# Optimization experiments

Measured on AMD Instinct MI355X. Metric: run time of the kernel, lower is better.

Reference implementation:

```python
import jax, jax.numpy as jnp
import numpy as np
import math

B, H, L, DK = 4, 12, 1024, 64
GLOBAL, LOCAL, INIT_VAL = 8, 4, 8
W = INIT_VAL + 1  # window length fed to each GRU
MAX_VAL = 1.0e12


def setup_inputs() -> dict:
    k0 = jax.random.key(0)
    ks = jax.random.split(k0, 9)
    bound = 1.0 / math.sqrt(DK)
    uni = lambda k, shape: jax.random.uniform(k, shape, jnp.float32, -bound, bound)
    return {
        "query": jax.random.normal(ks[0], (B, H, L, DK), jnp.float32),
        "key": jax.random.normal(ks[1], (B, H, L, DK), jnp.float32),
        "value": jax.random.normal(ks[2], (B, H, L, DK), jnp.float32),
        "mask": jax.random.randint(ks[3], (B, 1, L, L), 0, 2, jnp.int32),
        # per-local-head GRU parameters (torch nn.GRU layout: gates [r, z, n])
        "w_ih": uni(ks[4], (LOCAL, 3 * DK, DK)),
        "w_hh": uni(ks[5], (LOCAL, 3 * DK, DK)),
        "b_ih": uni(ks[6], (LOCAL, 3 * DK)),
        "b_hh": uni(ks[7], (LOCAL, 3 * DK)),
    }


def reference(query, key, value, mask, w_ih, w_hh, b_ih, b_hh):
    b, h, l, d_k = query.shape
    # ---- global softmax-attention heads ----
    q_g, k_g, v_g = query[:, :GLOBAL], key[:, :GLOBAL], value[:, :GLOBAL]
    scores = jnp.einsum('bhqd,bhkd->bhqk', q_g, k_g) / math.sqrt(d_k)
    scores = jnp.where(mask == 0, -MAX_VAL, scores)
    p_attn = jax.nn.softmax(scores, axis=-1)
    out_g = jnp.einsum('bhqk,bhkd->bhqd', p_attn, v_g)  # (b, GLOBAL, l, d_k)

    # ---- local heads: windowed value gather ----
    v_l = value[:, GLOBAL:]                                   # (b, LOCAL, l, d_k)
    v_pad = jnp.pad(v_l, ((0, 0), (0, 0), (0, INIT_VAL), (0, 0)))
    dist = jnp.arange(l)[:, None] + jnp.arange(W)[None, :]    # (l, W) forward window
    v_aug = v_pad[:, :, dist, :]                              # (b, LOCAL, l, W, d_k)
    x = v_aug.reshape(b * LOCAL * l, W, d_k)                  # all windows, shared by every GRU

    # ---- per-head GRU over the window; keep last hidden state ----
    def gru_last_hidden(wih, whh, bih, bhh):
        xg = jnp.einsum('ntd,gd->ntg', x, wih) + bih          # (N, W, 3*d_k), input gates precomputed
        def step(hc, xg_t):
            gh = hc @ whh.T + bhh
            xr, xz, xn = jnp.split(xg_t, 3, axis=-1)
            hr, hz, hn = jnp.split(gh, 3, axis=-1)
            r = jax.nn.sigmoid(xr + hr)
            z = jax.nn.sigmoid(xz + hz)
            n_ = jnp.tanh(xn + r * hn)
            return (1.0 - z) * n_ + z * hc, None
        h0 = jnp.zeros((x.shape[0], d_k), x.dtype)
        hT, _ = jax.lax.scan(step, h0, jnp.swapaxes(xg, 0, 1))
        return hT                                             # (N, d_k)

    hs = jax.vmap(gru_last_hidden)(w_ih, w_hh, b_ih, b_hh)    # (LOCAL, N, d_k)
    # faithful to torch cat: GRU i applied to ALL local heads -> LOCAL*LOCAL output heads
    out_l = hs.reshape(LOCAL, b, LOCAL, l, d_k).transpose(1, 0, 2, 3, 4)
    out_l = out_l.reshape(b, LOCAL * LOCAL, l, d_k)

    return jnp.concatenate([out_g, out_l], axis=1)            # (b, GLOBAL + LOCAL^2, l, d_k)
```

## Files before the change

kernel.cpp:

```cpp
#include <hip/hip_runtime.h>

#define B_  4
#define H_  12
#define L_  1024
#define DK_ 64
#define GH_ 8
#define WS_ 9

#define ATTN_LDS_BYTES (3 * 64 * 64 * 2)
#define GRU_W_OFF   0
#define GRU_XG_OFF  24576
#define GRU_HB_OFF  81024
#define GRU_BIH_OFF 113792
#define GRU_LDS_BYTES 114560

#define MB_WORDS (B_ * L_ * 16)

typedef __attribute__((ext_vector_type(8))) short short8;
typedef __attribute__((ext_vector_type(4))) float f32x4;

#define MFMA_BF16(a, b, c) __builtin_amdgcn_mfma_f32_16x16x32_bf16((a), (b), (c), 0, 0, 0)

__device__ __forceinline__ unsigned short f2bf(float f) {
  unsigned int u = __builtin_bit_cast(unsigned int, f);
  u += 0x7fffu + ((u >> 16) & 1u);
  return (unsigned short)(u >> 16);
}
__device__ __forceinline__ float bf2f(unsigned short s) {
  return __builtin_bit_cast(float, ((unsigned int)s) << 16);
}
__device__ __forceinline__ short8 pack8(const float4 a, const float4 b) {
  short8 r;
  r[0] = (short)f2bf(a.x); r[1] = (short)f2bf(a.y);
  r[2] = (short)f2bf(a.z); r[3] = (short)f2bf(a.w);
  r[4] = (short)f2bf(b.x); r[5] = (short)f2bf(b.y);
  r[6] = (short)f2bf(b.z); r[7] = (short)f2bf(b.w);
  return r;
}
__device__ __forceinline__ uint4 packrow16(const float4 a, const float4 b) {
  uint4 r;
  r.x = (unsigned)f2bf(a.x) | ((unsigned)f2bf(a.y) << 16);
  r.y = (unsigned)f2bf(a.z) | ((unsigned)f2bf(a.w) << 16);
  r.z = (unsigned)f2bf(b.x) | ((unsigned)f2bf(b.y) << 16);
  r.w = (unsigned)f2bf(b.z) | ((unsigned)f2bf(b.w) << 16);
  return r;
}

__global__ __launch_bounds__(256) void maskpack_kernel(
    const int* __restrict__ mask, unsigned long long* __restrict__ mb)
{
  const int idx = blockIdx.x * 256 + threadIdx.x;
  const int* src = mask + (size_t)idx * 64;
  unsigned long long bits = 0ull;
#pragma unroll
  for (int i = 0; i < 16; ++i) {
    const int4 m4 = *(const int4*)(src + i * 4);
    if (m4.x) bits |= 1ull << (i * 4 + 0);
    if (m4.y) bits |= 1ull << (i * 4 + 1);
    if (m4.z) bits |= 1ull << (i * 4 + 2);
    if (m4.w) bits |= 1ull << (i * 4 + 3);
  }
  mb[idx] = bits;
}

__global__ __launch_bounds__(256) void attn_kernel(
    const float* __restrict__ q, const float* __restrict__ k,
    const float* __restrict__ v, const int* __restrict__ mask,
    const unsigned long long* __restrict__ mb, const int use_bits,
    float* __restrict__ out)
{
  extern __shared__ char smc[];
  char* sK  = smc;
  char* sVT = smc + 8192;
  char* sP  = smc + 16384;

  const int tid = threadIdx.x;
  const int q0 = blockIdx.x * 64;
  const int h  = blockIdx.y;
  const int b  = blockIdx.z;

  const int w  = tid >> 6;
  const int ln = tid & 63;
  const int lg = ln >> 4;
  const int c  = ln & 15;

  const size_t hbase = ((size_t)b * H_ + h) * L_ * DK_;
  const float* kp = k + hbase;
  const float* vp = v + hbase;
  const int*   mp = mask + (size_t)b * L_ * L_;
  const unsigned long long* mbp = mb + (size_t)b * L_ * 16;

  short8 qa[2];
  {
    const float* qrow = q + hbase + (size_t)(q0 + w * 16 + c) * DK_ + lg * 8;
#pragma unroll
    for (int kt = 0; kt < 2; ++kt) {
      const float4 f0 = *(const float4*)(qrow + kt * 32);
      const float4 f1 = *(const float4*)(qrow + kt * 32 + 4);
      qa[kt] = pack8(f0, f1);
    }
  }

  char* sPw = sP + w * 2048;

  f32x4 o_[4];
#pragma unroll
  for (int nt = 0; nt < 4; ++nt) { o_[nt][0] = 0.f; o_[nt][1] = 0.f; o_[nt][2] = 0.f; o_[nt][3] = 0.f; }
  float mrun[4], lrun[4];
#pragma unroll
  for (int r = 0; r < 4; ++r) { mrun[r] = -1e30f; lrun[r] = 0.f; }

  const int rr  = tid >> 2;
  const int c16 = (tid & 3) << 4;

  for (int kt0 = 0; kt0 < 16; ++kt0) {
    {
      const float* ksrc = kp + (size_t)(kt0 * 64 + rr) * DK_ + c16;
      const float4 k0 = *(const float4*)(ksrc);
      const float4 k1 = *(const float4*)(ksrc + 4);
      const float4 k2 = *(const float4*)(ksrc + 8);
      const float4 k3 = *(const float4*)(ksrc + 12);
      const int kb = rr * 128 + c16 * 2;
      const int sw = (rr & 7) << 4;
      *(uint4*)(sK + ((kb) ^ sw))      = packrow16(k0, k1);
      *(uint4*)(sK + ((kb + 16) ^ sw)) = packrow16(k2, k3);

      const float* vsrc = vp + (size_t)(kt0 * 64 + rr) * DK_ + c16;
      const float4 v0 = *(const float4*)(vsrc);
      const float4 v1 = *(const float4*)(vsrc + 4);
      const float4 v2 = *(const float4*)(vsrc + 8);
      const float4 v3 = *(const float4*)(vsrc + 12);
      const float vv[16] = {v0.x, v0.y, v0.z, v0.w, v1.x, v1.y, v1.z, v1.w,
                            v2.x, v2.y, v2.z, v2.w, v3.x, v3.y, v3.z, v3.w};
#pragma unroll
      for (int j = 0; j < 16; ++j) {
        const int d = c16 + j;
        *(unsigned short*)(sVT + ((d * 128 + rr * 2) ^ ((d & 7) << 4))) = f2bf(vv[j]);
      }
    }
    __syncthreads();

    f32x4 acc[4];
#pragma unroll
    for (int nt = 0; nt < 4; ++nt) {
      acc[nt][0] = 0.f; acc[nt][1] = 0.f; acc[nt][2] = 0.f; acc[nt][3] = 0.f;
#pragma unroll
      for (int kt = 0; kt < 2; ++kt) {
        const int off = (((nt * 16 + c) * 128 + kt * 64 + lg * 16) ^ ((c & 7) << 4));
        const short8 bk = __builtin_bit_cast(short8, *(const uint4*)(sK + off));
        acc[nt] = MFMA_BF16(qa[kt], bk, acc[nt]);
      }
    }

#pragma unroll
    for (int r = 0; r < 4; ++r) {
      const int qr = q0 + w * 16 + lg * 4 + r;
      unsigned long long mword = 0ull;
      int mi0 = 0, mi1 = 0, mi2 = 0, mi3 = 0;
      if (use_bits) {
        mword = mbp[(size_t)qr * 16 + kt0];
      } else {
        const int* mrow = mp + (size_t)qr * L_ + kt0 * 64 + c;
        mi0 = mrow[0]; mi1 = mrow[16]; mi2 = mrow[32]; mi3 = mrow[48];
      }
      const bool k0_ = use_bits ? ((mword >> (c)) & 1ull)      : (mi0 != 0);
      const bool k1_ = use_bits ? ((mword >> (16 + c)) & 1ull) : (mi1 != 0);
      const bool k2_ = use_bits ? ((mword >> (32 + c)) & 1ull) : (mi2 != 0);
      const bool k3_ = use_bits ? ((mword >> (48 + c)) & 1ull) : (mi3 != 0);
      const float s0_ = k0_ ? acc[0][r] * 0.125f : -1e12f;
      const float s1_ = k1_ ? acc[1][r] * 0.125f : -1e12f;
      const float s2_ = k2_ ? acc[2][r] * 0.125f : -1e12f;
      const float s3_ = k3_ ? acc[3][r] * 0.125f : -1e12f;
      float mt = fmaxf(fmaxf(s0_, s1_), fmaxf(s2_, s3_));
#pragma unroll
      for (int off = 1; off < 16; off <<= 1) mt = fmaxf(mt, __shfl_xor(mt, off));
      const float mnew = fmaxf(mrun[r], mt);
      const float p0 = __expf(s0_ - mnew);
      const float p1 = __expf(s1_ - mnew);
      const float p2 = __expf(s2_ - mnew);
      const float p3 = __expf(s3_ - mnew);
      float pt = p0 + p1 + p2 + p3;
#pragma unroll
      for (int off = 1; off < 16; off <<= 1) pt += __shfl_xor(pt, off);
      const float scale = __expf(mrun[r] - mnew);
      mrun[r] = mnew;
      lrun[r] = lrun[r] * scale + pt;
      o_[0][r] *= scale; o_[1][r] *= scale; o_[2][r] *= scale; o_[3][r] *= scale;
      const int prow = lg * 4 + r;
      const int pb = prow * 128;
      const int psw = (prow & 7) << 4;
      *(unsigned short*)(sPw + ((pb + (c * 2)) ^ psw))       = f2bf(p0);
      *(unsigned short*)(sPw + ((pb + (16 + c) * 2) ^ psw))  = f2bf(p1);
      *(unsigned short*)(sPw + ((pb + (32 + c) * 2) ^ psw))  = f2bf(p2);
      *(unsigned short*)(sPw + ((pb + (48 + c) * 2) ^ psw))  = f2bf(p3);
    }

#pragma unroll
    for (int kt = 0; kt < 2; ++kt) {
      const int aoff = ((c * 128 + kt * 64 + lg * 16) ^ ((c & 7) << 4));
      const short8 pa = __builtin_bit_cast(short8, *(const uint4*)(sPw + aoff));
#pragma unroll
      for (int nt = 0; nt < 4; ++nt) {
        const int boff = (((nt * 16 + c) * 128 + kt * 64 + lg * 16) ^ ((c & 7) << 4));
        const short8 bv = __builtin_bit_cast(short8, *(const uint4*)(sVT + boff));
        o_[nt] = MFMA_BF16(pa, bv, o_[nt]);
      }
    }
    __syncthreads();
  }

  float* op = out + (((size_t)b * 24 + h) * L_ + q0 + w * 16) * DK_;
#pragma unroll
  for (int r = 0; r < 4; ++r) {
    const float inv = 1.f / lrun[r];
#pragma unroll
    for (int nt = 0; nt < 4; ++nt)
      op[(size_t)(lg * 4 + r) * DK_ + nt * 16 + c] = o_[nt][r] * inv;
  }
}

__global__ __launch_bounds__(512) void gru_kernel(
    const float* __restrict__ value, const float* __restrict__ wih_g,
    const float* __restrict__ whh_g, const float* __restrict__ bih_g,
    const float* __restrict__ bhh_g, float* __restrict__ out)
{
  extern __shared__ char smc[];
  char*           sW   = smc + GRU_W_OFF;
  unsigned short* sXG  = (unsigned short*)(smc + GRU_XG_OFF);
  char*           sHB  = smc + GRU_HB_OFF;
  float*          sBih = (float*)(smc + GRU_BIH_OFF);

  const int tid  = threadIdx.x;
  const int l0   = blockIdx.x * 128;
  const int gset = blockIdx.y >> 2;
  const int vh   = blockIdx.y & 3;
  const int b    = blockIdx.z;

  const float* vp   = value + (((size_t)b * H_ + GH_ + vh) * L_) * DK_;
  const float* wih  = wih_g + (size_t)gset * 192 * DK_;
  const float* whh  = whh_g + (size_t)gset * 192 * DK_;
  const float* bihp = bih_g + gset * 192;
  const float* bhhp = bhh_g + gset * 192;

  if (tid < 192) sBih[tid] = bihp[tid];
#pragma unroll
  for (int k2 = 0; k2 < 4; ++k2) {
    uint4 z; z.x = 0u; z.y = 0u; z.z = 0u; z.w = 0u;
    *(uint4*)(sHB + ((size_t)tid + 512 * k2) * 16) = z;
  }
  for (int cid = tid; cid < 1536; cid += 512) {
    const int row = cid >> 3, ch = cid & 7;
    const float* wp = whh + row * 64 + ch * 8;
    const float4 w0 = *(const float4*)wp;
    const float4 w1 = *(const float4*)(wp + 4);
    *(uint4*)(sW + ((row * 128 + ch * 16) ^ ((row & 7) << 4))) = packrow16(w0, w1);
  }
  __syncthreads();

  const int w  = tid >> 6;
  const int ln = tid & 63;
  const int lg = ln >> 4;
  const int c  = ln & 15;

  for (int t = w; t < 108; t += 8) {
    const int Mt = t / 12, Nt = t - Mt * 12;
    const int row = l0 + Mt * 16 + c;
    const bool valid = row < L_;
    const float* va = vp + (size_t)row * 64 + lg * 8;
    float4 z4; z4.x = 0.f; z4.y = 0.f; z4.z = 0.f; z4.w = 0.f;
    const float4 a00 = valid ? *(const float4*)(va)      : z4;
    const float4 a01 = valid ? *(const float4*)(va + 4)  : z4;
    const float4 a10 = valid ? *(const float4*)(va + 32) : z4;
    const float4 a11 = valid ? *(const float4*)(va + 36) : z4;
    const float* wb = wih + (size_t)(Nt * 16 + c) * 64 + lg * 8;
    const float4 b00 = *(const float4*)(wb);
    const float4 b01 = *(const float4*)(wb + 4);
    const float4 b10 = *(const float4*)(wb + 32);
    const float4 b11 = *(const float4*)(wb + 36);
    f32x4 acc = {0.f, 0.f, 0.f, 0.f};
    acc = MFMA_BF16(pack8(a00, a01), pack8(b00, b01), acc);
    acc = MFMA_BF16(pack8(a10, a11), pack8(b10, b11), acc);
    const float bias = sBih[Nt * 16 + c];
    const int pos0 = Mt * 16 + lg * 4;
    const int jj = Nt * 16 + c;
#pragma unroll
    for (int r = 0; r < 4; ++r)
      sXG[(pos0 + r) * 196 + jj] = f2bf(acc[r] + bias);
  }
  __syncthreads();

  char* hbH = sHB + w * 4096;
  char* hbL = hbH + 2048;

  float bhh[12];
#pragma unroll
  for (int n = 0; n < 12; ++n) bhh[n] = bhhp[n * 16 + c];

  f32x4 hfr[4];
#pragma unroll
  for (int t = 0; t < 4; ++t) { hfr[t][0] = 0.f; hfr[t][1] = 0.f; hfr[t][2] = 0.f; hfr[t][3] = 0.f; }

  const int seqB = w * 16;

  for (int ts = 0; ts < WS_; ++ts) {
    short8 ahi[2], alo[2];
#pragma unroll
    for (int kt = 0; kt < 2; ++kt) {
      const int ao = (c * 128 + kt * 64 + lg * 16) ^ ((c & 7) << 4);
      ahi[kt] = __builtin_bit_cast(short8, *(const uint4*)(hbH + ao));
      alo[kt] = __builtin_bit_cast(short8, *(const uint4*)(hbL + ao));
    }
    f32x4 acc[12];
#pragma unroll
    for (int n = 0; n < 12; ++n) {
      acc[n][0] = 0.f; acc[n][1] = 0.f; acc[n][2] = 0.f; acc[n][3] = 0.f;
#pragma unroll
      for (int kt = 0; kt < 2; ++kt) {
        const int wo = ((n * 16 + c) * 128 + kt * 64 + lg * 16) ^ ((c & 7) << 4);
        const short8 bw = __builtin_bit_cast(short8, *(const uint4*)(sW + wo));
        acc[n] = MFMA_BF16(ahi[kt], bw, acc[n]);
        acc[n] = MFMA_BF16(alo[kt], bw, acc[n]);
      }
    }
#pragma unroll
    for (int t = 0; t < 4; ++t) {
#pragma unroll
      for (int r = 0; r < 4; ++r) {
        const int pos = seqB + lg * 4 + r + ts;
        const int d = c + 16 * t;
        const float xr = bf2f(sXG[pos * 196 + d]);
        const float xz = bf2f(sXG[pos * 196 + 64 + d]);
        const float xn = bf2f(sXG[pos * 196 + 128 + d]);
        const float ghr = acc[t][r] + bhh[t];
        const float ghz = acc[t + 4][r] + bhh[t + 4];
        const float ghn = acc[t + 8][r] + bhh[t + 8];
        const float rr = __builtin_amdgcn_rcpf(1.f + __expf(-(xr + ghr)));
        const float zz = __builtin_amdgcn_rcpf(1.f + __expf(-(xz + ghz)));
        const float e2 = __expf(2.f * (xn + rr * ghn));
        const float nn = 1.f - 2.f * __builtin_amdgcn_rcpf(1.f + e2);
        float h = hfr[t][r];
        h = (1.f - zz) * nn + zz * h;
        hfr[t][r] = h;
        const int sl = lg * 4 + r;
        const int hb = (sl * 128 + d * 2) ^ ((sl & 7) << 4);
        const unsigned short hhi = f2bf(h);
        *(unsigned short*)(hbH + hb) = hhi;
        *(unsigned short*)(hbL + hb) = f2bf(h - bf2f(hhi));
      }
    }
  }

  float* op = out + (((size_t)b * 24 + (GH_ + gset * 4 + vh)) * L_ + l0) * DK_;
#pragma unroll
  for (int t = 0; t < 4; ++t)
#pragma unroll
    for (int r = 0; r < 4; ++r)
      op[(size_t)(seqB + lg * 4 + r) * 64 + c + 16 * t] = hfr[t][r];
}

extern "C" void kernel_launch(void* const* d_in, const int* in_sizes, int n_in,
                              void* d_out, int out_size, void* d_ws, size_t ws_size,
                              hipStream_t stream) {
  (void)in_sizes; (void)n_in; (void)out_size;
  const float* q   = (const float*)d_in[0];
  const float* k   = (const float*)d_in[1];
  const float* v   = (const float*)d_in[2];
  const int*   msk = (const int*)d_in[3];
  const float* wih = (const float*)d_in[4];
  const float* whh = (const float*)d_in[5];
  const float* bih = (const float*)d_in[6];
  const float* bhh = (const float*)d_in[7];
  float* out = (float*)d_out;

  const int use_bits = (ws_size >= (size_t)MB_WORDS * 8) ? 1 : 0;
  unsigned long long* mb = (unsigned long long*)d_ws;

  (void)hipFuncSetAttribute((const void*)gru_kernel,
                            hipFuncAttributeMaxDynamicSharedMemorySize, GRU_LDS_BYTES);

  if (use_bits)
    maskpack_kernel<<<dim3(MB_WORDS / 256), dim3(256), 0, stream>>>(msk, mb);
  attn_kernel<<<dim3(L_ / 64, GH_, B_), dim3(256), ATTN_LDS_BYTES, stream>>>(
      q, k, v, msk, mb, use_bits, out);
  gru_kernel<<<dim3(L_ / 128, 16, B_), dim3(512), GRU_LDS_BYTES, stream>>>(
      v, wih, whh, bih, bhh, out);
}
```

Measured before the change: 342.2 us.

## Prefetch next K/V/mask tile in attention and register-cache GRU input gates

In the attention kernel, the K, V and mask-bit loads for the next key tile are issued into registers right after the barrier, so global latency overlaps the MFMA and softmax work of the current tile. In the GRU kernel, the precomputed input-gate buffer is stored transposed (gate-major, packed bf16 pairs), and each lane loads its whole window slice into registers once before a fully unrolled time loop, replacing per-step scalar LDS reads. This adds register pressure (about 72 extra dwords of input gates per lane in the GRU, plus the prefetch registers in attention), which may lower occupancy.

```diff
diff --git a/kernel.cpp b/kernel.cpp
--- a/kernel.cpp
+++ b/kernel.cpp
@@ -8,11 +8,12 @@
 #define WS_ 9
 
 #define ATTN_LDS_BYTES (3 * 64 * 64 * 2)
-#define GRU_W_OFF   0
-#define GRU_XG_OFF  24576
-#define GRU_HB_OFF  81024
-#define GRU_BIH_OFF 113792
-#define GRU_LDS_BYTES 114560
+#define GRU_W_OFF    0
+#define GRU_XGT_OFF  24576
+#define GRU_HB_OFF   81408
+#define GRU_BIH_OFF  114176
+#define GRU_LDS_BYTES 114944
+#define XGT_STRIDE   296
 
 #define MB_WORDS (B_ * L_ * 16)
 
@@ -44,6 +45,11 @@
   r.z = (unsigned)f2bf(b.x) | ((unsigned)f2bf(b.y) << 16);
   r.w = (unsigned)f2bf(b.z) | ((unsigned)f2bf(b.w) << 16);
   return r;
+}
+__device__ __forceinline__ float xg_get(const uint2* xg3, const int wi) {
+  const unsigned d = (wi & 2) ? xg3[wi >> 2].y : xg3[wi >> 2].x;
+  return (wi & 1) ? __builtin_bit_cast(float, d & 0xffff0000u)
+                  : __builtin_bit_cast(float, d << 16);
 }
 
 __global__ __launch_bounds__(256) void maskpack_kernel(
@@ -113,25 +119,32 @@
   const int rr  = tid >> 2;
   const int c16 = (tid & 3) << 4;
 
+  float4 kreg[4], vreg[4];
+  unsigned long long mreg[4];
+  {
+    const float* ksrc = kp + (size_t)rr * DK_ + c16;
+    kreg[0] = *(const float4*)(ksrc);      kreg[1] = *(const float4*)(ksrc + 4);
+    kreg[2] = *(const float4*)(ksrc + 8);  kreg[3] = *(const float4*)(ksrc + 12);
+    const float* vsrc = vp + (size_t)rr * DK_ + c16;
+    vreg[0] = *(const float4*)(vsrc);      vreg[1] = *(const float4*)(vsrc + 4);
+    vreg[2] = *(const float4*)(vsrc + 8);  vreg[3] = *(const float4*)(vsrc + 12);
+    if (use_bits) {
+#pragma unroll
+      for (int r = 0; r < 4; ++r)
+        mreg[r] = mbp[(size_t)(q0 + w * 16 + lg * 4 + r) * 16 + 0];
+    }
+  }
+
   for (int kt0 = 0; kt0 < 16; ++kt0) {
     {
-      const float* ksrc = kp + (size_t)(kt0 * 64 + rr) * DK_ + c16;
-      const float4 k0 = *(const float4*)(ksrc);
-      const float4 k1 = *(const float4*)(ksrc + 4);
-      const float4 k2 = *(const float4*)(ksrc + 8);
-      const float4 k3 = *(const float4*)(ksrc + 12);
       const int kb = rr * 128 + c16 * 2;
       const int sw = (rr & 7) << 4;
-      *(uint4*)(sK + ((kb) ^ sw))      = packrow16(k0, k1);
-      *(uint4*)(sK + ((kb + 16) ^ sw)) = packrow16(k2, k3);
-
-      const float* vsrc = vp + (size_t)(kt0 * 64 + rr) * DK_ + c16;
-      const float4 v0 = *(const float4*)(vsrc);
-      const float4 v1 = *(const float4*)(vsrc + 4);
-      const float4 v2 = *(const float4*)(vsrc + 8);
-      const float4 v3 = *(const float4*)(vsrc + 12);
-      const float vv[16] = {v0.x, v0.y, v0.z, v0.w, v1.x, v1.y, v1.z, v1.w,
-                            v2.x, v2.y, v2.z, v2.w, v3.x, v3.y, v3.z, v3.w};
+      *(uint4*)(sK + ((kb) ^ sw))      = packrow16(kreg[0], kreg[1]);
+      *(uint4*)(sK + ((kb + 16) ^ sw)) = packrow16(kreg[2], kreg[3]);
+      const float vv[16] = {vreg[0].x, vreg[0].y, vreg[0].z, vreg[0].w,
+                            vreg[1].x, vreg[1].y, vreg[1].z, vreg[1].w,
+                            vreg[2].x, vreg[2].y, vreg[2].z, vreg[2].w,
+                            vreg[3].x, vreg[3].y, vreg[3].z, vreg[3].w};
 #pragma unroll
       for (int j = 0; j < 16; ++j) {
         const int d = c16 + j;
@@ -139,6 +152,24 @@
       }
     }
     __syncthreads();
+
+    unsigned long long mcur[4];
+#pragma unroll
+    for (int r = 0; r < 4; ++r) mcur[r] = mreg[r];
+    {
+      const int ktn = (kt0 + 1) & 15;
+      const float* ksrc = kp + (size_t)(ktn * 64 + rr) * DK_ + c16;
+      kreg[0] = *(const float4*)(ksrc);      kreg[1] = *(const float4*)(ksrc + 4);
+      kreg[2] = *(const float4*)(ksrc + 8);  kreg[3] = *(const float4*)(ksrc + 12);
+      const float* vsrc = vp + (size_t)(ktn * 64 + rr) * DK_ + c16;
+      vreg[0] = *(const float4*)(vsrc);      vreg[1] = *(const float4*)(vsrc + 4);
+      vreg[2] = *(const float4*)(vsrc + 8);  vreg[3] = *(const float4*)(vsrc + 12);
+      if (use_bits) {
+#pragma unroll
+        for (int r = 0; r < 4; ++r)
+          mreg[r] = mbp[(size_t)(q0 + w * 16 + lg * 4 + r) * 16 + ktn];
+      }
+    }
 
     f32x4 acc[4];
 #pragma unroll
@@ -154,19 +185,18 @@
 
 #pragma unroll
     for (int r = 0; r < 4; ++r) {
-      const int qr = q0 + w * 16 + lg * 4 + r;
-      unsigned long long mword = 0ull;
-      int mi0 = 0, mi1 = 0, mi2 = 0, mi3 = 0;
+      bool k0_, k1_, k2_, k3_;
       if (use_bits) {
-        mword = mbp[(size_t)qr * 16 + kt0];
+        const unsigned long long mword = mcur[r];
+        k0_ = (mword >> (c)) & 1ull;
+        k1_ = (mword >> (16 + c)) & 1ull;
+        k2_ = (mword >> (32 + c)) & 1ull;
+        k3_ = (mword >> (48 + c)) & 1ull;
       } else {
+        const int qr = q0 + w * 16 + lg * 4 + r;
         const int* mrow = mp + (size_t)qr * L_ + kt0 * 64 + c;
-        mi0 = mrow[0]; mi1 = mrow[16]; mi2 = mrow[32]; mi3 = mrow[48];
-      }
-      const bool k0_ = use_bits ? ((mword >> (c)) & 1ull)      : (mi0 != 0);
-      const bool k1_ = use_bits ? ((mword >> (16 + c)) & 1ull) : (mi1 != 0);
-      const bool k2_ = use_bits ? ((mword >> (32 + c)) & 1ull) : (mi2 != 0);
-      const bool k3_ = use_bits ? ((mword >> (48 + c)) & 1ull) : (mi3 != 0);
+        k0_ = mrow[0] != 0; k1_ = mrow[16] != 0; k2_ = mrow[32] != 0; k3_ = mrow[48] != 0;
+      }
       const float s0_ = k0_ ? acc[0][r] * 0.125f : -1e12f;
       const float s1_ = k1_ ? acc[1][r] * 0.125f : -1e12f;
       const float s2_ = k2_ ? acc[2][r] * 0.125f : -1e12f;
@@ -225,10 +255,10 @@
     const float* __restrict__ bhh_g, float* __restrict__ out)
 {
   extern __shared__ char smc[];
-  char*           sW   = smc + GRU_W_OFF;
-  unsigned short* sXG  = (unsigned short*)(smc + GRU_XG_OFF);
-  char*           sHB  = smc + GRU_HB_OFF;
-  float*          sBih = (float*)(smc + GRU_BIH_OFF);
+  char*  sW   = smc + GRU_W_OFF;
+  char*  sXGT = smc + GRU_XGT_OFF;
+  char*  sHB  = smc + GRU_HB_OFF;
+  float* sBih = (float*)(smc + GRU_BIH_OFF);
 
   const int tid  = threadIdx.x;
   const int l0   = blockIdx.x * 128;
@@ -283,25 +313,38 @@
     const float bias = sBih[Nt * 16 + c];
     const int pos0 = Mt * 16 + lg * 4;
     const int jj = Nt * 16 + c;
-#pragma unroll
-    for (int r = 0; r < 4; ++r)
-      sXG[(pos0 + r) * 196 + jj] = f2bf(acc[r] + bias);
+    uint2 pk;
+    pk.x = (unsigned)f2bf(acc[0] + bias) | ((unsigned)f2bf(acc[1] + bias) << 16);
+    pk.y = (unsigned)f2bf(acc[2] + bias) | ((unsigned)f2bf(acc[3] + bias) << 16);
+    *(uint2*)(sXGT + jj * XGT_STRIDE + pos0 * 2) = pk;
   }
   __syncthreads();
 
   char* hbH = sHB + w * 4096;
   char* hbL = hbH + 2048;
+  const int seqB = w * 16;
 
   float bhh[12];
 #pragma unroll
   for (int n = 0; n < 12; ++n) bhh[n] = bhhp[n * 16 + c];
 
+  const int P0 = seqB + lg * 4;
+  uint2 xgq[4][3][3];
+#pragma unroll
+  for (int t = 0; t < 4; ++t)
+#pragma unroll
+    for (int g = 0; g < 3; ++g) {
+      const char* rowp = sXGT + (g * 64 + t * 16 + c) * XGT_STRIDE + P0 * 2;
+#pragma unroll
+      for (int kk = 0; kk < 3; ++kk)
+        xgq[t][g][kk] = *(const uint2*)(rowp + kk * 8);
+    }
+
   f32x4 hfr[4];
 #pragma unroll
   for (int t = 0; t < 4; ++t) { hfr[t][0] = 0.f; hfr[t][1] = 0.f; hfr[t][2] = 0.f; hfr[t][3] = 0.f; }
 
-  const int seqB = w * 16;
-
+#pragma unroll
   for (int ts = 0; ts < WS_; ++ts) {
     short8 ahi[2], alo[2];
 #pragma unroll
@@ -326,11 +369,10 @@
     for (int t = 0; t < 4; ++t) {
 #pragma unroll
       for (int r = 0; r < 4; ++r) {
-        const int pos = seqB + lg * 4 + r + ts;
-        const int d = c + 16 * t;
-        const float xr = bf2f(sXG[pos * 196 + d]);
-        const float xz = bf2f(sXG[pos * 196 + 64 + d]);
-        const float xn = bf2f(sXG[pos * 196 + 128 + d]);
+        const int wi = r + ts;
+        const float xr = xg_get(xgq[t][0], wi);
+        const float xz = xg_get(xgq[t][1], wi);
+        const float xn = xg_get(xgq[t][2], wi);
         const float ghr = acc[t][r] + bhh[t];
         const float ghz = acc[t + 4][r] + bhh[t + 4];
         const float ghn = acc[t + 8][r] + bhh[t + 8];
@@ -342,6 +384,7 @@
         h = (1.f - zz) * nn + zz * h;
         hfr[t][r] = h;
         const int sl = lg * 4 + r;
+        const int d = c + 16 * t;
         const int hb = (sl * 128 + d * 2) ^ ((sl & 7) << 4);
         const unsigned short hhi = f2bf(h);
         *(unsigned short*)(hbH + hb) = hhi;
```

After: 325.9 us. 4.8% less time.
